# Optimization experiments

Hardware: AMD Instinct MI355X
Metric: run time of the kernel (lower is better)

The kernel has to match this reference:

```python
import jax, jax.numpy as jnp
import numpy as np

B, T, V, S = 64, 200, 20000, 1


def setup_inputs() -> dict:
    key = jax.random.key(0)
    k1, k2, k3, k4 = jax.random.split(key, 4)
    output = jax.random.normal(k1, (B, T, V), dtype=jnp.float32)
    labels = jax.random.randint(k2, (B, T), 0, V, dtype=jnp.int64)
    x_lens = jax.random.randint(k3, (B,), 1, T + 1, dtype=jnp.int32)  # lengths >= 1
    uids = jnp.arange(B, dtype=jnp.int64)[:, None]
    neg_ids = jax.random.randint(k4, (B, T, S), 0, V, dtype=jnp.int64)
    return {"output": output, "labels": labels, "x_lens": x_lens,
            "uids": uids, "neg_ids": neg_ids}


def reference(output, labels, x_lens, uids, neg_ids):
    # output: [B, T, V]; labels: [B, T]; x_lens: [B]; neg_ids: [B, T, S]
    b, t, v = output.shape
    s = neg_ids.shape[-1]
    # pos[b, i, j] = output[b, i, labels[b, j]]  (slice + advanced index -> [L, L])
    pos = jnp.take_along_axis(output, labels[:, None, :], axis=2)          # [B, T, T]
    # neg[b, i, j, k] = output[b, i, neg_ids[b, j, k]]
    neg = jnp.take_along_axis(output, neg_ids.reshape(b, 1, t * s), axis=2)
    neg = neg.reshape(b, t, t, s)                                          # [B, T, T, S]
    diff = pos[..., None] - neg                                            # [B, T, T, S]
    ls = jax.nn.log_sigmoid(diff)
    mask = jnp.arange(t)[None, :] < x_lens[:, None]                        # [B, T]
    valid = (mask[:, :, None] & mask[:, None, :]).astype(ls.dtype)[..., None]
    lens_f = x_lens.astype(ls.dtype)
    counts = lens_f * lens_f * s                                           # L^2 * S per sample
    per_sample = -(ls * valid).sum(axis=(1, 2, 3)) / counts                # mean over valid block
    return per_sample.sum()[None]  # shape (1,), matching FloatTensor accumulator
```

## Files before the change

### kernel.cpp

```cpp
#include <hip/hip_runtime.h>


#define BB 64
#define TT 200
#define VV 20000
#define NBLK (BB * TT)

__global__ __launch_bounds__(64) void bpr_partial_kernel(
    const float* __restrict__ output,
    const int*   __restrict__ labels,
    const int*   __restrict__ x_lens,
    const int*   __restrict__ neg_ids,
    float*       __restrict__ partial)
{
    const int blk = blockIdx.x;
    const int b = blk / TT;
    const int i = blk - b * TT;
    const int L = x_lens[b];
    const int lane = threadIdx.x;

    float sum = 0.0f;
    if (i < L) {
        const float* __restrict__ row = output + ((size_t)b * TT + i) * VV;
        const int*   __restrict__ lab = labels  + b * TT;
        const int*   __restrict__ neg = neg_ids + b * TT;
        for (int j = lane; j < L; j += 64) {
            const float xp = row[lab[j]];
            const float xn = row[neg[j]];
            const float d  = xp - xn;
            sum += fminf(d, 0.0f) - log1pf(__expf(-fabsf(d)));
        }
    }

    #pragma unroll
    for (int off = 32; off > 0; off >>= 1)
        sum += __shfl_down(sum, off, 64);

    if (lane == 0) {
        const float Lf = (float)L;
        partial[blk] = -sum / (Lf * Lf);
    }
}

__global__ __launch_bounds__(1024) void bpr_reduce_kernel(
    const float* __restrict__ partial, float* __restrict__ out)
{
    float s = 0.0f;
    for (int k = threadIdx.x; k < NBLK; k += 1024)
        s += partial[k];

    __shared__ float wsum[16];
    #pragma unroll
    for (int off = 32; off > 0; off >>= 1)
        s += __shfl_down(s, off, 64);
    if ((threadIdx.x & 63) == 0) wsum[threadIdx.x >> 6] = s;
    __syncthreads();

    if (threadIdx.x < 64) {
        float v = (threadIdx.x < 16) ? wsum[threadIdx.x] : 0.0f;
        #pragma unroll
        for (int off = 32; off > 0; off >>= 1)
            v += __shfl_down(v, off, 64);
        if (threadIdx.x == 0) out[0] = v;
    }
}

extern "C" void kernel_launch(void* const* d_in, const int* in_sizes, int n_in,
                              void* d_out, int out_size, void* d_ws, size_t ws_size,
                              hipStream_t stream) {
    const float* output  = (const float*)d_in[0];
    const int*   labels  = (const int*)d_in[1];
    const int*   x_lens  = (const int*)d_in[2];
    const int*   neg_ids = (const int*)d_in[4];
    float* partial = (float*)d_ws;
    float* result  = (float*)d_out;

    bpr_partial_kernel<<<NBLK, 64, 0, stream>>>(output, labels, x_lens, neg_ids, partial);
    bpr_reduce_kernel<<<1, 1024, 0, stream>>>(partial, result);
}
```

Measured before the change: 1.109 ms.

## Stage full output row in LDS via float4 loads before gathering

Each valid (b,i) row is now copied in full (20000 floats, 80KB) into shared memory with coalesced float4 loads by a 1024-thread block. The positive and negative values are then gathered from LDS, with one thread per j. The aim is to replace scattered global gathers, which were latency bound, with streaming bandwidth-bound reads. The cost is reading whole rows rather than only the touched elements, plus a large LDS footprint that limits occupancy and relies on gfx950's larger LDS.

After: 1.171 ms. 5.6% more time.

```diff
diff --git a/kernel.cpp b/kernel.cpp
--- a/kernel.cpp
+++ b/kernel.cpp
@@ -5,40 +5,61 @@
 #define TT 200
 #define VV 20000
 #define NBLK (BB * TT)
+#define NT 1024
 
-__global__ __launch_bounds__(64) void bpr_partial_kernel(
+__global__ __launch_bounds__(NT) void bpr_partial_kernel(
     const float* __restrict__ output,
     const int*   __restrict__ labels,
     const int*   __restrict__ x_lens,
     const int*   __restrict__ neg_ids,
     float*       __restrict__ partial)
 {
+    __shared__ float row_s[VV];
+    __shared__ float wsum[NT / 64];
+
     const int blk = blockIdx.x;
-    const int b = blk / TT;
-    const int i = blk - b * TT;
-    const int L = x_lens[b];
-    const int lane = threadIdx.x;
+    const int b   = blk / TT;
+    const int i   = blk - b * TT;
+    const int L   = x_lens[b];
+    const int tid = threadIdx.x;
 
     float sum = 0.0f;
     if (i < L) {
-        const float* __restrict__ row = output + ((size_t)b * TT + i) * VV;
-        const int*   __restrict__ lab = labels  + b * TT;
-        const int*   __restrict__ neg = neg_ids + b * TT;
-        for (int j = lane; j < L; j += 64) {
-            const float xp = row[lab[j]];
-            const float xn = row[neg[j]];
+        const float4* __restrict__ src =
+            reinterpret_cast<const float4*>(output + ((size_t)b * TT + i) * VV);
+        float4* dst = reinterpret_cast<float4*>(row_s);
+        #pragma unroll
+        for (int k = 0; k < 5; ++k) {
+            const int idx = tid + k * NT;
+            if (idx < VV / 4) dst[idx] = src[idx];
+        }
+        __syncthreads();
+
+        if (tid < L) {
+            const int* __restrict__ lab = labels  + b * TT;
+            const int* __restrict__ neg = neg_ids + b * TT;
+            const float xp = row_s[lab[tid]];
+            const float xn = row_s[neg[tid]];
             const float d  = xp - xn;
-            sum += fminf(d, 0.0f) - log1pf(__expf(-fabsf(d)));
+            sum = fminf(d, 0.0f) - log1pf(__expf(-fabsf(d)));
         }
     }
 
     #pragma unroll
     for (int off = 32; off > 0; off >>= 1)
         sum += __shfl_down(sum, off, 64);
+    if ((tid & 63) == 0) wsum[tid >> 6] = sum;
+    __syncthreads();
 
-    if (lane == 0) {
-        const float Lf = (float)L;
-        partial[blk] = -sum / (Lf * Lf);
+    if (tid < 64) {
+        float v = (tid < 16) ? wsum[tid] : 0.0f;
+        #pragma unroll
+        for (int off = 32; off > 0; off >>= 1)
+            v += __shfl_down(v, off, 64);
+        if (tid == 0) {
+            const float Lf = (float)L;
+            partial[blk] = -v / (Lf * Lf);
+        }
     }
 }
 
@@ -75,6 +96,6 @@
     float* partial = (float*)d_ws;
     float* result  = (float*)d_out;
 
-    bpr_partial_kernel<<<NBLK, 64, 0, stream>>>(output, labels, x_lens, neg_ids, partial);
+    bpr_partial_kernel<<<NBLK, NT, 0, stream>>>(output, labels, x_lens, neg_ids, partial);
     bpr_reduce_kernel<<<1, 1024, 0, stream>>>(partial, result);
 }
```
